# Kernel optimization log

Hardware: AMD Instinct MI355X
Metric: run time of the kernel (lower is better)

The kernel has to match this reference:

```python
import jax, jax.numpy as jnp
import numpy as np

B, S, DIM = 2, 2048, 2048
N_HEADS, N_KV_HEADS = 16, 4
HEAD_DIM = DIM // N_HEADS  # 128
N_REP = N_HEADS // N_KV_HEADS  # 4


def setup_inputs() -> dict:
    key = jax.random.key(0)
    ks = jax.random.split(key, 7)
    x = jax.random.normal(ks[0], (B, S, DIM), dtype=jnp.float32)
    cos = jax.random.uniform(ks[1], (S, HEAD_DIM // 2), dtype=jnp.float32)
    sin = jax.random.uniform(ks[2], (S, HEAD_DIM // 2), dtype=jnp.float32)
    sc = 1.0 / np.sqrt(DIM)
    wq = jax.random.normal(ks[3], (DIM, N_HEADS * HEAD_DIM), dtype=jnp.float32) * sc
    wk = jax.random.normal(ks[4], (DIM, N_KV_HEADS * HEAD_DIM), dtype=jnp.float32) * sc
    wv = jax.random.normal(ks[5], (DIM, N_KV_HEADS * HEAD_DIM), dtype=jnp.float32) * sc
    wo = jax.random.normal(ks[6], (N_HEADS * HEAD_DIM, DIM), dtype=jnp.float32) * sc
    return {"x": x, "cos": cos, "sin": sin, "wq": wq, "wk": wk, "wv": wv, "wo": wo}


def _rope(t, cos, sin):
    # t: [B, S, H, hd]; cos/sin: [S, hd/2] -> broadcast as [1, S, 1, hd/2]
    tr, ti = t[..., ::2], t[..., 1::2]
    c = cos[None, :, None, :]
    s = sin[None, :, None, :]
    out_r = tr * c - ti * s
    out_i = tr * s + ti * c
    # interleave back: stack on new last axis then flatten
    return jnp.stack([out_r, out_i], axis=-1).reshape(t.shape)


def reference(x, cos, sin, wq, wk, wv, wo):
    bsz, seqlen, _ = x.shape
    xq = (x @ wq).reshape(bsz, seqlen, N_HEADS, HEAD_DIM)
    xk = (x @ wk).reshape(bsz, seqlen, N_KV_HEADS, HEAD_DIM)
    xv = (x @ wv).reshape(bsz, seqlen, N_KV_HEADS, HEAD_DIM)
    xq = _rope(xq, cos, sin)
    xk = _rope(xk, cos, sin)
    # GQA: repeat kv heads -> [B, S, H, hd]
    xk = jnp.repeat(xk, N_REP, axis=2)
    xv = jnp.repeat(xv, N_REP, axis=2)
    scale = 1.0 / jnp.sqrt(jnp.asarray(HEAD_DIM, dtype=x.dtype))
    scores = jnp.einsum("bqhd,bkhd->bhqk", xq, xk) * scale
    causal = jnp.tril(jnp.ones((seqlen, seqlen), dtype=bool))
    scores = jnp.where(causal[None, None, :, :], scores, jnp.asarray(-jnp.inf, dtype=scores.dtype))
    attn = jax.nn.softmax(scores, axis=-1)
    out = jnp.einsum("bhqk,bkhd->bqhd", attn, xv)
    out = out.reshape(bsz, seqlen, N_HEADS * HEAD_DIM)
    return out @ wo
```

## Files before the change

### kernel.cpp

```cpp
#include <hip/hip_runtime.h>
#include <stdint.h>

#define SEQ 2048

typedef uint16_t u16;
typedef uint32_t u32;
typedef __attribute__((ext_vector_type(4))) float f32x4;
typedef __attribute__((ext_vector_type(8))) __bf16 bf16x8;
typedef __attribute__((ext_vector_type(4))) __bf16 bf16x4;

__device__ __forceinline__ u16 f2bf(float f) {
    u32 u = __float_as_uint(f);
    u += 0x7FFFu + ((u >> 16) & 1u);
    return (u16)(u >> 16);
}
__device__ __forceinline__ float bf2f(u16 h) {
    return __uint_as_float(((u32)h) << 16);
}
__device__ __forceinline__ void async16(const void* g, void* l) {
    auto gp = (__attribute__((address_space(1))) void*)const_cast<void*>(g);
    auto lp = (__attribute__((address_space(3))) void*)l;
    __builtin_amdgcn_global_load_lds(gp, lp, 16, 0, 0);
}

__global__ __launch_bounds__(256) void convert_bf16(const float* __restrict__ src,
                                                    u16* __restrict__ dst) {
    int i = blockIdx.x * 256 + threadIdx.x;
    float4 v = ((const float4*)src)[i];
    u32 lo = (u32)f2bf(v.x) | ((u32)f2bf(v.y) << 16);
    u32 hi = (u32)f2bf(v.z) | ((u32)f2bf(v.w) << 16);
    ((uint2*)dst)[i] = make_uint2(lo, hi);
}

__global__ __launch_bounds__(256) void tconv(const float* __restrict__ src,
                                             u16* __restrict__ dst, int N, int K) {
    __shared__ float tile[64][65];
    const int n0 = blockIdx.x * 64, k0 = blockIdx.y * 64;
    const int tid = threadIdx.x;
#pragma unroll
    for (int p = 0; p < 4; p++) {
        int r = p * 16 + (tid >> 4);
        int c = (tid & 15) * 4;
        float4 v = *(const float4*)&src[(size_t)(k0 + r) * N + n0 + c];
        tile[r][c] = v.x; tile[r][c+1] = v.y; tile[r][c+2] = v.z; tile[r][c+3] = v.w;
    }
    __syncthreads();
#pragma unroll
    for (int p = 0; p < 4; p++) {
        int n = p * 16 + (tid >> 4);
        int kq = (tid & 15) * 4;
        u32 lo = (u32)f2bf(tile[kq+0][n]) | ((u32)f2bf(tile[kq+1][n]) << 16);
        u32 hi = (u32)f2bf(tile[kq+2][n]) | ((u32)f2bf(tile[kq+3][n]) << 16);
        *(uint2*)&dst[(size_t)(n0 + n) * K + k0 + kq] = make_uint2(lo, hi);
    }
}

template <bool F32OUT>
__global__ __launch_bounds__(256) void gemm128(const u16* __restrict__ A,
                                               const u16* __restrict__ Bt,
                                               void* __restrict__ Cv,
                                               int M, int N, int K) {
    __shared__ u16 lA[128 * 32];
    __shared__ u16 lB[128 * 32];
    const int tid = threadIdx.x;
    const int m0 = blockIdx.y * 128, n0 = blockIdx.x * 128;
    const int lane = tid & 63;
    const int lr = lane & 15, quad = lane >> 4;
    const int w = tid >> 6;
    const int wm = (w >> 1) * 64, wn = (w & 1) * 64;

    f32x4 acc[4][4] = {};

    const int srow = tid >> 2;
    const int schunk = (tid & 3) ^ (srow & 3);
    const u16* aS0 = A  + (size_t)(m0 + srow) * K + schunk * 8;
    const u16* aS1 = aS0 + (size_t)64 * K;
    const u16* bS0 = Bt + (size_t)(n0 + srow) * K + schunk * 8;
    const u16* bS1 = bS0 + (size_t)64 * K;
    u16* lAd = lA + tid * 8;
    u16* lBd = lB + tid * 8;

    for (int k0 = 0; k0 < K; k0 += 32) {
        __syncthreads();
        async16(aS0 + k0, lAd);
        async16(aS1 + k0, lAd + 2048);
        async16(bS0 + k0, lBd);
        async16(bS1 + k0, lBd + 2048);
        __syncthreads();
        bf16x8 af[4], bfr[4];
        const int cs = (quad ^ (lr & 3)) * 8;
#pragma unroll
        for (int i = 0; i < 4; i++)
            af[i] = *(const bf16x8*)&lA[(wm + i * 16 + lr) * 32 + cs];
#pragma unroll
        for (int i = 0; i < 4; i++)
            bfr[i] = *(const bf16x8*)&lB[(wn + i * 16 + lr) * 32 + cs];
#pragma unroll
        for (int mf = 0; mf < 4; mf++)
#pragma unroll
            for (int nf = 0; nf < 4; nf++)
                acc[mf][nf] = __builtin_amdgcn_mfma_f32_16x16x32_bf16(
                    af[mf], bfr[nf], acc[mf][nf], 0, 0, 0);
    }

#pragma unroll
    for (int mf = 0; mf < 4; mf++) {
#pragma unroll
        for (int nf = 0; nf < 4; nf++) {
#pragma unroll
            for (int r = 0; r < 4; r++) {
                size_t row = (size_t)(m0 + wm + mf * 16 + quad * 4 + r);
                size_t col = (size_t)(n0 + wn + nf * 16 + lr);
                if (F32OUT)
                    ((float*)Cv)[row * (size_t)N + col] = acc[mf][nf][r];
                else
                    ((u16*)Cv)[row * (size_t)N + col] = f2bf(acc[mf][nf][r]);
            }
        }
    }
}

__global__ __launch_bounds__(256) void rope_k(u16* __restrict__ qkv,
                                              const float* __restrict__ cosp,
                                              const float* __restrict__ sinp) {
    const int t = blockIdx.x;
    const int spos = t & (SEQ - 1);
    const int tid = threadIdx.x;
    u16* row = qkv + (size_t)t * 3072;
    const int col = 2048 + 2 * tid;
    const int ci = tid & 63;
    u32 v = *(u32*)(row + col);
    float tr = bf2f((u16)(v & 0xFFFFu));
    float ti = bf2f((u16)(v >> 16));
    float cs = cosp[spos * 64 + ci];
    float sn = sinp[spos * 64 + ci];
    float orr = tr * cs - ti * sn;
    float oi  = tr * sn + ti * cs;
    *(u32*)(row + col) = (u32)f2bf(orr) | ((u32)f2bf(oi) << 16);
}

__global__ __launch_bounds__(256) void transpose_v(const u16* __restrict__ qkv,
                                                   u16* __restrict__ vt) {
    __shared__ u16 tile[64][65];
    const int bid = blockIdx.x;
    const int dt = bid & 1;
    const int st = (bid >> 1) & 31;
    const int kh = (bid >> 6) & 3;
    const int b  = bid >> 8;
    const int tid = threadIdx.x;
#pragma unroll
    for (int pp = 0; pp < 2; pp++) {
        int r  = pp * 32 + (tid >> 3);
        int c8 = (tid & 7) * 8;
        const u16* src = qkv + (size_t)(b * SEQ + st * 64 + r) * 3072 + 2560 + kh * 128 + dt * 64 + c8;
        uint4 v = *(const uint4*)src;
        tile[r][c8+0] = (u16)(v.x & 0xFFFF); tile[r][c8+1] = (u16)(v.x >> 16);
        tile[r][c8+2] = (u16)(v.y & 0xFFFF); tile[r][c8+3] = (u16)(v.y >> 16);
        tile[r][c8+4] = (u16)(v.z & 0xFFFF); tile[r][c8+5] = (u16)(v.z >> 16);
        tile[r][c8+6] = (u16)(v.w & 0xFFFF); tile[r][c8+7] = (u16)(v.w >> 16);
    }
    __syncthreads();
#pragma unroll
    for (int pp = 0; pp < 2; pp++) {
        int dr = pp * 32 + (tid >> 3);
        int s8 = (tid & 7) * 8;
        uint4 o;
        o.x = (u32)tile[s8+0][dr] | ((u32)tile[s8+1][dr] << 16);
        o.y = (u32)tile[s8+2][dr] | ((u32)tile[s8+3][dr] << 16);
        o.z = (u32)tile[s8+4][dr] | ((u32)tile[s8+5][dr] << 16);
        o.w = (u32)tile[s8+6][dr] | ((u32)tile[s8+7][dr] << 16);
        u16* dst = vt + ((size_t)((b * 4 + kh) * 128 + dt * 64 + dr)) * SEQ + st * 64 + s8;
        *(uint4*)dst = o;
    }
}

__global__ __launch_bounds__(512, 2) void flash_attn(const u16* __restrict__ qkv,
                                                     const u16* __restrict__ vt,
                                                     const float* __restrict__ cosp,
                                                     const float* __restrict__ sinp,
                                                     u16* __restrict__ ob) {
    __shared__ u16 sh[49152];
    const int bidx = blockIdx.x;
    const int a  = bidx & 7;
    const int bh = bidx >> 3;
    const int b = bh >> 4, h = bh & 15, kh = h >> 2;
    const int tid = threadIdx.x;
    const int w = tid >> 6, lane = tid & 63;
    const int grp = w >> 2, wl = w & 3;
    const int lr = lane & 15, quad = lane >> 4;
    const float qscale = 0.088388347762f * 1.4426950408889634f;

    u16* lKg = sh + grp * 16384;
    u16* lVg = lKg + 8192;
    u16* lPw = sh + 32768 + w * 2048;

    const int tidg = tid & 255;
    const int krow = tidg >> 4;
    const int kchunk = (tidg & 15) ^ krow;
    const int vrow = tidg >> 3;
    const int vchunk = (tidg & 7) ^ (vrow & 7);
    const u16* kRow = qkv + (size_t)b * SEQ * 3072 + 2048 + kh * 128
                    + (size_t)krow * 3072 + kchunk * 8;
    const u16* vRow = vt + (size_t)(b * 4 + kh) * 128 * SEQ
                    + (size_t)vrow * SEQ + vchunk * 8;
    u16* lKd = lKg + tidg * 8;
    u16* lVd = lVg + tidg * 8;

    float* mO = (float*)sh;
    float* mM = (float*)(sh + 32768);

    for (int p = 0; p < 2; p++) {
        const int qt = p ? (7 - a) : (8 + a);
        const int niters = p ? (8 - a) : (9 + a);
        const int kt0 = grp * niters;

        bf16x8 qf[2][4];
#pragma unroll
        for (int qi = 0; qi < 2; qi++) {
            const int token = qt * 128 + wl * 32 + qi * 16 + lr;
            const u16* qb = qkv + (size_t)(b * SEQ + token) * 3072 + h * 128;
#pragma unroll
            for (int kk = 0; kk < 4; kk++) {
                uint4 raw = *(const uint4*)(qb + kk * 32 + quad * 8);
                u32 rw[4] = {raw.x, raw.y, raw.z, raw.w};
                union { u16 us[8]; bf16x8 v; } fr;
#pragma unroll
                for (int pp = 0; pp < 4; pp++) {
                    int ci = kk * 16 + quad * 4 + pp;
                    float cv = cosp[token * 64 + ci];
                    float sv = sinp[token * 64 + ci];
                    float tr = bf2f((u16)(rw[pp] & 0xFFFFu));
                    float ti = bf2f((u16)(rw[pp] >> 16));
                    fr.us[2 * pp]     = f2bf((tr * cv - ti * sv) * qscale);
                    fr.us[2 * pp + 1] = f2bf((tr * sv + ti * cv) * qscale);
                }
                qf[qi][kk] = fr.v;
            }
        }

        f32x4 o[2][8] = {};
        float m_st[2] = {-1e30f, -1e30f};
        float l_st[2] = {0.f, 0.f};
        const int qg = qt * 128 + wl * 32 + lr;

        for (int t = 0; t < niters; t++) {
            const int kt = kt0 + t;
#pragma unroll
            for (int i = 0; i < 4; i++)
                async16(kRow + (size_t)(kt * 64 + i * 16) * 3072, lKd + i * 2048);
#pragma unroll
            for (int i = 0; i < 4; i++)
                async16(vRow + (size_t)(i * 32) * SEQ + kt * 64, lVd + i * 2048);
            asm volatile("s_waitcnt vmcnt(0)" ::: "memory");
            asm volatile("s_barrier" ::: "memory");

            f32x4 sc[2][4] = {};
#pragma unroll
            for (int nf = 0; nf < 4; nf++) {
#pragma unroll
                for (int kk = 0; kk < 4; kk++) {
                    bf16x8 ak = *(const bf16x8*)&lKg[(nf * 16 + lr) * 128 + (((kk * 4 + quad) ^ lr) * 8)];
                    sc[0][nf] = __builtin_amdgcn_mfma_f32_16x16x32_bf16(ak, qf[0][kk], sc[0][nf], 0, 0, 0);
                    sc[1][nf] = __builtin_amdgcn_mfma_f32_16x16x32_bf16(ak, qf[1][kk], sc[1][nf], 0, 0, 0);
                }
            }

            const int kb = kt * 64 + quad * 4;
#pragma unroll
            for (int qi = 0; qi < 2; qi++) {
                float ps[4][4];
                float mnew = m_st[qi];
                const int qrow_g = qg + qi * 16;
#pragma unroll
                for (int nf = 0; nf < 4; nf++)
#pragma unroll
                    for (int r = 0; r < 4; r++) {
                        float v = sc[qi][nf][r];
                        if ((kb + nf * 16 + r) > qrow_g) v = -1e30f;
                        ps[nf][r] = v;
                        mnew = fmaxf(mnew, v);
                    }
                mnew = fmaxf(mnew, __shfl_xor(mnew, 16));
                mnew = fmaxf(mnew, __shfl_xor(mnew, 32));
                float rsum = 0.f;
#pragma unroll
                for (int nf = 0; nf < 4; nf++)
#pragma unroll
                    for (int r = 0; r < 4; r++) {
                        float e = exp2f(ps[nf][r] - mnew);
                        ps[nf][r] = e;
                        rsum += e;
                    }
                rsum += __shfl_xor(rsum, 16);
                rsum += __shfl_xor(rsum, 32);
                float alpha = exp2f(m_st[qi] - mnew);
                l_st[qi] = l_st[qi] * alpha + rsum;
                m_st[qi] = mnew;
#pragma unroll
                for (int r = 0; r < 4; r++) {
                    float ar = __shfl(alpha, quad * 4 + r, 16);
#pragma unroll
                    for (int nd = 0; nd < 8; nd++) o[qi][nd][r] *= ar;
                }
                const int qrow = qi * 16 + lr;
#pragma unroll
                for (int nf = 0; nf < 4; nf++) {
                    u32 lo = (u32)f2bf(ps[nf][0]) | ((u32)f2bf(ps[nf][1]) << 16);
                    u32 hi = (u32)f2bf(ps[nf][2]) | ((u32)f2bf(ps[nf][3]) << 16);
                    int c = (nf * 4 + quad) ^ lr;
                    *(uint2*)&lPw[qrow * 64 + c * 4] = make_uint2(lo, hi);
                }
            }

#pragma unroll
            for (int kf = 0; kf < 2; kf++) {
                bf16x8 pa[2];
#pragma unroll
                for (int qi = 0; qi < 2; qi++) {
                    int c0 = (kf * 8 + quad * 2) ^ lr;
                    int c1 = (kf * 8 + quad * 2 + 1) ^ lr;
                    bf16x4 p0 = *(const bf16x4*)&lPw[(qi * 16 + lr) * 64 + c0 * 4];
                    bf16x4 p1 = *(const bf16x4*)&lPw[(qi * 16 + lr) * 64 + c1 * 4];
                    pa[qi] = __builtin_shufflevector(p0, p1, 0, 1, 2, 3, 4, 5, 6, 7);
                }
#pragma unroll
                for (int nd = 0; nd < 8; nd++) {
                    bf16x8 vb = *(const bf16x8*)&lVg[(nd * 16 + lr) * 64 + (((kf * 4 + quad) ^ (lr & 7)) * 8)];
                    o[0][nd] = __builtin_amdgcn_mfma_f32_16x16x32_bf16(pa[0], vb, o[0][nd], 0, 0, 0);
                    o[1][nd] = __builtin_amdgcn_mfma_f32_16x16x32_bf16(pa[1], vb, o[1][nd], 0, 0, 0);
                }
            }

            asm volatile("s_barrier" ::: "memory");
        }

        __syncthreads();
        if (grp == 1) {
#pragma unroll
            for (int qi = 0; qi < 2; qi++) {
#pragma unroll
                for (int r = 0; r < 4; r++) {
                    int row = wl * 32 + qi * 16 + quad * 4 + r;
#pragma unroll
                    for (int nd = 0; nd < 8; nd++)
                        mO[row * 128 + nd * 16 + lr] = o[qi][nd][r];
                }
                if (quad == 0) {
                    int rowl = wl * 32 + qi * 16 + lr;
                    mM[rowl * 2]     = m_st[qi];
                    mM[rowl * 2 + 1] = l_st[qi];
                }
            }
        }
        __syncthreads();
        if (grp == 0) {
#pragma unroll
            for (int qi = 0; qi < 2; qi++) {
                int rowl = wl * 32 + qi * 16 + lr;
                float m1 = mM[rowl * 2], l1 = mM[rowl * 2 + 1];
                float M  = fmaxf(m_st[qi], m1);
                float a0 = exp2f(m_st[qi] - M);
                float a1 = exp2f(m1 - M);
                float li = 1.0f / (l_st[qi] * a0 + l1 * a1);
                u16* obase = ob + (size_t)(b * SEQ + qt * 128 + wl * 32 + qi * 16) * 2048 + h * 128;
#pragma unroll
                for (int r = 0; r < 4; r++) {
                    float a0b = __shfl(a0, quad * 4 + r, 16);
                    float a1b = __shfl(a1, quad * 4 + r, 16);
                    float lib = __shfl(li, quad * 4 + r, 16);
                    int row = wl * 32 + qi * 16 + quad * 4 + r;
#pragma unroll
                    for (int nd = 0; nd < 8; nd++) {
                        float val = (o[qi][nd][r] * a0b + mO[row * 128 + nd * 16 + lr] * a1b) * lib;
                        obase[(quad * 4 + r) * 2048 + nd * 16 + lr] = f2bf(val);
                    }
                }
            }
        }
        __syncthreads();
    }
}

extern "C" void kernel_launch(void* const* d_in, const int* in_sizes, int n_in,
                              void* d_out, int out_size, void* d_ws, size_t ws_size,
                              hipStream_t stream) {
    (void)in_sizes; (void)n_in; (void)out_size; (void)ws_size;
    const float* x    = (const float*)d_in[0];
    const float* cosp = (const float*)d_in[1];
    const float* sinp = (const float*)d_in[2];
    const float* wq   = (const float*)d_in[3];
    const float* wk   = (const float*)d_in[4];
    const float* wv   = (const float*)d_in[5];
    const float* wo   = (const float*)d_in[6];
    float* out = (float*)d_out;

    char* ws = (char*)d_ws;
    u16* xb    = (u16*)(ws);
    u16* qkvb  = (u16*)(ws + (size_t)16 * 1024 * 1024);
    u16* wqkvT = (u16*)(ws + (size_t)40 * 1024 * 1024);
    u16* woT   = (u16*)(ws + (size_t)52 * 1024 * 1024);
    u16* vtb   = (u16*)(ws + (size_t)60 * 1024 * 1024);
    u16* ob    = xb;

    convert_bf16<<<8192, 256, 0, stream>>>(x, xb);
    tconv<<<dim3(32, 32), 256, 0, stream>>>(wq, wqkvT, 2048, 2048);
    tconv<<<dim3( 8, 32), 256, 0, stream>>>(wk, wqkvT + (size_t)2048 * 2048, 512, 2048);
    tconv<<<dim3( 8, 32), 256, 0, stream>>>(wv, wqkvT + (size_t)2560 * 2048, 512, 2048);
    tconv<<<dim3(32, 32), 256, 0, stream>>>(wo, woT, 2048, 2048);
    gemm128<false><<<dim3(24, 32), 256, 0, stream>>>(xb, wqkvT, (void*)qkvb, 4096, 3072, 2048);
    rope_k<<<4096, 256, 0, stream>>>(qkvb, cosp, sinp);
    transpose_v<<<512, 256, 0, stream>>>(qkvb, vtb);
    flash_attn<<<256, 512, 0, stream>>>(qkvb, vtb, cosp, sinp, ob);
    gemm128<true><<<dim3(16, 32), 256, 0, stream>>>(ob, woT, (void*)out, 4096, 2048, 2048);
}
```

Baseline: 339.5 us.

## Fuse RoPE and V-transpose into QKV GEMM epilogue, double-buffer K in attention

Merges the four weight transpose-convert launches into one kernel. The QKV GEMM epilogue now applies RoPE (with the softmax scale folded into Q) and writes V transposed through LDS, which removes the rope_k and transpose_v kernels and the per-iteration Q RoPE in attention. The flash attention kernel double-buffers K tiles with async loads and staged waitcnts, and pads the merge buffer stride. This costs more LDS, drops occupancy to one block per CU, and the epilogue now loads cos/sin per element.

```diff
diff --git a/kernel.cpp b/kernel.cpp
--- a/kernel.cpp
+++ b/kernel.cpp
@@ -22,6 +22,8 @@
     auto lp = (__attribute__((address_space(3))) void*)l;
     __builtin_amdgcn_global_load_lds(gp, lp, 16, 0, 0);
 }
+
+#define QSCALE (0.088388347762f * 1.4426950408889634f)
 
 __global__ __launch_bounds__(256) void convert_bf16(const float* __restrict__ src,
                                                     u16* __restrict__ dst) {
@@ -32,10 +34,20 @@
     ((uint2*)dst)[i] = make_uint2(lo, hi);
 }
 
-__global__ __launch_bounds__(256) void tconv(const float* __restrict__ src,
-                                             u16* __restrict__ dst, int N, int K) {
+__global__ __launch_bounds__(256) void tconv_all(const float* __restrict__ wq,
+                                                 const float* __restrict__ wk,
+                                                 const float* __restrict__ wv,
+                                                 const float* __restrict__ wo,
+                                                 u16* __restrict__ wqkvT,
+                                                 u16* __restrict__ woT) {
     __shared__ float tile[64][65];
-    const int n0 = blockIdx.x * 64, k0 = blockIdx.y * 64;
+    const int nt = blockIdx.x, kt = blockIdx.y;
+    const float* src; u16* dst; int N, nloc;
+    if (nt < 32)      { src = wq; dst = wqkvT;                        N = 2048; nloc = nt; }
+    else if (nt < 40) { src = wk; dst = wqkvT + (size_t)2048 * 2048;  N = 512;  nloc = nt - 32; }
+    else if (nt < 48) { src = wv; dst = wqkvT + (size_t)2560 * 2048;  N = 512;  nloc = nt - 40; }
+    else              { src = wo; dst = woT;                          N = 2048; nloc = nt - 48; }
+    const int n0 = nloc * 64, k0 = kt * 64;
     const int tid = threadIdx.x;
 #pragma unroll
     for (int p = 0; p < 4; p++) {
@@ -51,17 +63,21 @@
         int kq = (tid & 15) * 4;
         u32 lo = (u32)f2bf(tile[kq+0][n]) | ((u32)f2bf(tile[kq+1][n]) << 16);
         u32 hi = (u32)f2bf(tile[kq+2][n]) | ((u32)f2bf(tile[kq+3][n]) << 16);
-        *(uint2*)&dst[(size_t)(n0 + n) * K + k0 + kq] = make_uint2(lo, hi);
+        *(uint2*)&dst[(size_t)(n0 + n) * 2048 + k0 + kq] = make_uint2(lo, hi);
     }
 }
 
-template <bool F32OUT>
+template <int MODE>
 __global__ __launch_bounds__(256) void gemm128(const u16* __restrict__ A,
                                                const u16* __restrict__ Bt,
                                                void* __restrict__ Cv,
+                                               u16* __restrict__ vt,
+                                               const float* __restrict__ cosp,
+                                               const float* __restrict__ sinp,
                                                int M, int N, int K) {
-    __shared__ u16 lA[128 * 32];
-    __shared__ u16 lB[128 * 32];
+    __shared__ u16 sh[(MODE == 2) ? 16384 : 8192];
+    u16* lA = sh;
+    u16* lB = sh + 4096;
     const int tid = threadIdx.x;
     const int m0 = blockIdx.y * 128, n0 = blockIdx.x * 128;
     const int lane = tid & 63;
@@ -103,83 +119,73 @@
                     af[mf], bfr[nf], acc[mf][nf], 0, 0, 0);
     }
 
-#pragma unroll
-    for (int mf = 0; mf < 4; mf++) {
-#pragma unroll
-        for (int nf = 0; nf < 4; nf++) {
-#pragma unroll
-            for (int r = 0; r < 4; r++) {
-                size_t row = (size_t)(m0 + wm + mf * 16 + quad * 4 + r);
-                size_t col = (size_t)(n0 + wn + nf * 16 + lr);
-                if (F32OUT)
+    if (MODE == 1) {
+#pragma unroll
+        for (int mf = 0; mf < 4; mf++)
+#pragma unroll
+            for (int nf = 0; nf < 4; nf++)
+#pragma unroll
+                for (int r = 0; r < 4; r++) {
+                    size_t row = (size_t)(m0 + wm + mf * 16 + quad * 4 + r);
+                    size_t col = (size_t)(n0 + wn + nf * 16 + lr);
                     ((float*)Cv)[row * (size_t)N + col] = acc[mf][nf][r];
-                else
-                    ((u16*)Cv)[row * (size_t)N + col] = f2bf(acc[mf][nf][r]);
+                }
+    } else {
+        const int ncol0 = n0 + wn;
+        if (ncol0 < 2560) {
+            const float s2 = (ncol0 < 2048) ? QSCALE : 1.0f;
+#pragma unroll
+            for (int mf = 0; mf < 4; mf++) {
+                const int tokb = m0 + wm + mf * 16 + quad * 4;
+#pragma unroll
+                for (int nf = 0; nf < 4; nf++) {
+                    const int ci = (((ncol0 & 127) + nf * 16 + lr) >> 1);
+#pragma unroll
+                    for (int r = 0; r < 4; r++) {
+                        int tok = tokb + r;
+                        int spos = tok & (SEQ - 1);
+                        float cv = cosp[spos * 64 + ci] * s2;
+                        float sv = sinp[spos * 64 + ci] * s2;
+                        float val = acc[mf][nf][r];
+                        float par = __shfl_xor(val, 1);
+                        float outv = (lane & 1) ? fmaf(par, sv, val * cv)
+                                                : fmaf(val, cv, -par * sv);
+                        ((u16*)Cv)[(size_t)tok * 3072 + ncol0 + nf * 16 + lr] = f2bf(outv);
+                    }
+                }
+            }
+        } else {
+            __syncthreads();
+            u16* tr = sh + w * 4096;
+#pragma unroll
+            for (int mf = 0; mf < 4; mf++)
+#pragma unroll
+                for (int nf = 0; nf < 4; nf++)
+#pragma unroll
+                    for (int r = 0; r < 4; r++) {
+                        int row  = mf * 16 + quad * 4 + r;
+                        int colL = nf * 16 + lr;
+                        tr[colL * 64 + ((row + 8 * colL) & 63)] = f2bf(acc[mf][nf][r]);
+                    }
+            const int b = m0 >> 11;
+            const int s0base = (m0 & 2047) + wm;
+#pragma unroll
+            for (int i = 0; i < 8; i++) {
+                int dL = i * 8 + (lane >> 3);
+                int t0 = (lane & 7) * 8;
+                uint4 v = *(const uint4*)&tr[dL * 64 + ((t0 + 8 * dL) & 63)];
+                int dglob = (ncol0 - 2560) + dL;
+                int khh = dglob >> 7, dh = dglob & 127;
+                *(uint4*)&vt[((size_t)((b * 4 + khh) * 128 + dh)) * SEQ + s0base + t0] = v;
             }
         }
     }
 }
 
-__global__ __launch_bounds__(256) void rope_k(u16* __restrict__ qkv,
-                                              const float* __restrict__ cosp,
-                                              const float* __restrict__ sinp) {
-    const int t = blockIdx.x;
-    const int spos = t & (SEQ - 1);
-    const int tid = threadIdx.x;
-    u16* row = qkv + (size_t)t * 3072;
-    const int col = 2048 + 2 * tid;
-    const int ci = tid & 63;
-    u32 v = *(u32*)(row + col);
-    float tr = bf2f((u16)(v & 0xFFFFu));
-    float ti = bf2f((u16)(v >> 16));
-    float cs = cosp[spos * 64 + ci];
-    float sn = sinp[spos * 64 + ci];
-    float orr = tr * cs - ti * sn;
-    float oi  = tr * sn + ti * cs;
-    *(u32*)(row + col) = (u32)f2bf(orr) | ((u32)f2bf(oi) << 16);
-}
-
-__global__ __launch_bounds__(256) void transpose_v(const u16* __restrict__ qkv,
-                                                   u16* __restrict__ vt) {
-    __shared__ u16 tile[64][65];
-    const int bid = blockIdx.x;
-    const int dt = bid & 1;
-    const int st = (bid >> 1) & 31;
-    const int kh = (bid >> 6) & 3;
-    const int b  = bid >> 8;
-    const int tid = threadIdx.x;
-#pragma unroll
-    for (int pp = 0; pp < 2; pp++) {
-        int r  = pp * 32 + (tid >> 3);
-        int c8 = (tid & 7) * 8;
-        const u16* src = qkv + (size_t)(b * SEQ + st * 64 + r) * 3072 + 2560 + kh * 128 + dt * 64 + c8;
-        uint4 v = *(const uint4*)src;
-        tile[r][c8+0] = (u16)(v.x & 0xFFFF); tile[r][c8+1] = (u16)(v.x >> 16);
-        tile[r][c8+2] = (u16)(v.y & 0xFFFF); tile[r][c8+3] = (u16)(v.y >> 16);
-        tile[r][c8+4] = (u16)(v.z & 0xFFFF); tile[r][c8+5] = (u16)(v.z >> 16);
-        tile[r][c8+6] = (u16)(v.w & 0xFFFF); tile[r][c8+7] = (u16)(v.w >> 16);
-    }
-    __syncthreads();
-#pragma unroll
-    for (int pp = 0; pp < 2; pp++) {
-        int dr = pp * 32 + (tid >> 3);
-        int s8 = (tid & 7) * 8;
-        uint4 o;
-        o.x = (u32)tile[s8+0][dr] | ((u32)tile[s8+1][dr] << 16);
-        o.y = (u32)tile[s8+2][dr] | ((u32)tile[s8+3][dr] << 16);
-        o.z = (u32)tile[s8+4][dr] | ((u32)tile[s8+5][dr] << 16);
-        o.w = (u32)tile[s8+6][dr] | ((u32)tile[s8+7][dr] << 16);
-        u16* dst = vt + ((size_t)((b * 4 + kh) * 128 + dt * 64 + dr)) * SEQ + st * 64 + s8;
-        *(uint4*)dst = o;
-    }
-}
-
-__global__ __launch_bounds__(512, 2) void flash_attn(const u16* __restrict__ qkv,
+__global__ __launch_bounds__(512, 1) void flash_attn(const u16* __restrict__ qkv,
                                                      const u16* __restrict__ vt,
-                                                     const float* __restrict__ cosp,
-                                                     const float* __restrict__ sinp,
                                                      u16* __restrict__ ob) {
-    __shared__ u16 sh[49152];
+    __shared__ u16 sh[65536];
     const int bidx = blockIdx.x;
     const int a  = bidx & 7;
     const int bh = bidx >> 3;
@@ -188,11 +194,11 @@
     const int w = tid >> 6, lane = tid & 63;
     const int grp = w >> 2, wl = w & 3;
     const int lr = lane & 15, quad = lane >> 4;
-    const float qscale = 0.088388347762f * 1.4426950408889634f;
-
-    u16* lKg = sh + grp * 16384;
-    u16* lVg = lKg + 8192;
-    u16* lPw = sh + 32768 + w * 2048;
+
+    u16* kb0 = sh + grp * 24576;
+    u16* kb1 = kb0 + 8192;
+    u16* lVg = kb0 + 16384;
+    u16* lPw = sh + 49152 + w * 2048;
 
     const int tidg = tid & 255;
     const int krow = tidg >> 4;
@@ -203,11 +209,10 @@
                     + (size_t)krow * 3072 + kchunk * 8;
     const u16* vRow = vt + (size_t)(b * 4 + kh) * 128 * SEQ
                     + (size_t)vrow * SEQ + vchunk * 8;
-    u16* lKd = lKg + tidg * 8;
     u16* lVd = lVg + tidg * 8;
 
     float* mO = (float*)sh;
-    float* mM = (float*)(sh + 32768);
+    float* mM = (float*)(sh + 49152);
 
     for (int p = 0; p < 2; p++) {
         const int qt = p ? (7 - a) : (8 + a);
@@ -217,25 +222,10 @@
         bf16x8 qf[2][4];
 #pragma unroll
         for (int qi = 0; qi < 2; qi++) {
-            const int token = qt * 128 + wl * 32 + qi * 16 + lr;
-            const u16* qb = qkv + (size_t)(b * SEQ + token) * 3072 + h * 128;
-#pragma unroll
-            for (int kk = 0; kk < 4; kk++) {
-                uint4 raw = *(const uint4*)(qb + kk * 32 + quad * 8);
-                u32 rw[4] = {raw.x, raw.y, raw.z, raw.w};
-                union { u16 us[8]; bf16x8 v; } fr;
-#pragma unroll
-                for (int pp = 0; pp < 4; pp++) {
-                    int ci = kk * 16 + quad * 4 + pp;
-                    float cv = cosp[token * 64 + ci];
-                    float sv = sinp[token * 64 + ci];
-                    float tr = bf2f((u16)(rw[pp] & 0xFFFFu));
-                    float ti = bf2f((u16)(rw[pp] >> 16));
-                    fr.us[2 * pp]     = f2bf((tr * cv - ti * sv) * qscale);
-                    fr.us[2 * pp + 1] = f2bf((tr * sv + ti * cv) * qscale);
-                }
-                qf[qi][kk] = fr.v;
-            }
+            const u16* qb = qkv + (size_t)(b * SEQ + qt * 128 + wl * 32 + qi * 16 + lr) * 3072 + h * 128;
+#pragma unroll
+            for (int kk = 0; kk < 4; kk++)
+                qf[qi][kk] = *(const bf16x8*)(qb + kk * 32 + quad * 8);
         }
 
         f32x4 o[2][8] = {};
@@ -243,29 +233,43 @@
         float l_st[2] = {0.f, 0.f};
         const int qg = qt * 128 + wl * 32 + lr;
 
+        {
+            u16* d = kb0 + tidg * 8;
+#pragma unroll
+            for (int i = 0; i < 4; i++)
+                async16(kRow + (size_t)(kt0 * 64 + i * 16) * 3072, d + i * 2048);
+        }
+
         for (int t = 0; t < niters; t++) {
             const int kt = kt0 + t;
 #pragma unroll
             for (int i = 0; i < 4; i++)
-                async16(kRow + (size_t)(kt * 64 + i * 16) * 3072, lKd + i * 2048);
-#pragma unroll
-            for (int i = 0; i < 4; i++)
                 async16(vRow + (size_t)(i * 32) * SEQ + kt * 64, lVd + i * 2048);
-            asm volatile("s_waitcnt vmcnt(0)" ::: "memory");
+            if (t + 1 < niters) {
+                u16* d = ((t + 1) & 1 ? kb1 : kb0) + tidg * 8;
+#pragma unroll
+                for (int i = 0; i < 4; i++)
+                    async16(kRow + (size_t)((kt + 1) * 64 + i * 16) * 3072, d + i * 2048);
+                asm volatile("s_waitcnt vmcnt(8)" ::: "memory");
+            } else {
+                asm volatile("s_waitcnt vmcnt(4)" ::: "memory");
+            }
             asm volatile("s_barrier" ::: "memory");
 
+            const u16* lKc = (t & 1) ? kb1 : kb0;
+
             f32x4 sc[2][4] = {};
 #pragma unroll
             for (int nf = 0; nf < 4; nf++) {
 #pragma unroll
                 for (int kk = 0; kk < 4; kk++) {
-                    bf16x8 ak = *(const bf16x8*)&lKg[(nf * 16 + lr) * 128 + (((kk * 4 + quad) ^ lr) * 8)];
+                    bf16x8 ak = *(const bf16x8*)&lKc[(nf * 16 + lr) * 128 + (((kk * 4 + quad) ^ lr) * 8)];
                     sc[0][nf] = __builtin_amdgcn_mfma_f32_16x16x32_bf16(ak, qf[0][kk], sc[0][nf], 0, 0, 0);
                     sc[1][nf] = __builtin_amdgcn_mfma_f32_16x16x32_bf16(ak, qf[1][kk], sc[1][nf], 0, 0, 0);
                 }
             }
 
-            const int kb = kt * 64 + quad * 4;
+            const int kb_ = kt * 64 + quad * 4;
 #pragma unroll
             for (int qi = 0; qi < 2; qi++) {
                 float ps[4][4];
@@ -276,7 +280,7 @@
 #pragma unroll
                     for (int r = 0; r < 4; r++) {
                         float v = sc[qi][nf][r];
-                        if ((kb + nf * 16 + r) > qrow_g) v = -1e30f;
+                        if ((kb_ + nf * 16 + r) > qrow_g) v = -1e30f;
                         ps[nf][r] = v;
                         mnew = fmaxf(mnew, v);
                     }
@@ -312,6 +316,10 @@
                 }
             }
 
+            if (t + 1 < niters) asm volatile("s_waitcnt vmcnt(4)" ::: "memory");
+            else                asm volatile("s_waitcnt vmcnt(0)" ::: "memory");
+            asm volatile("s_barrier" ::: "memory");
+
 #pragma unroll
             for (int kf = 0; kf < 2; kf++) {
                 bf16x8 pa[2];
@@ -343,7 +351,7 @@
                     int row = wl * 32 + qi * 16 + quad * 4 + r;
 #pragma unroll
                     for (int nd = 0; nd < 8; nd++)
-                        mO[row * 128 + nd * 16 + lr] = o[qi][nd][r];
+                        mO[row * 132 + nd * 16 + lr] = o[qi][nd][r];
                 }
                 if (quad == 0) {
                     int rowl = wl * 32 + qi * 16 + lr;
@@ -371,7 +379,7 @@
                     int row = wl * 32 + qi * 16 + quad * 4 + r;
 #pragma unroll
                     for (int nd = 0; nd < 8; nd++) {
-                        float val = (o[qi][nd][r] * a0b + mO[row * 128 + nd * 16 + lr] * a1b) * lib;
+                        float val = (o[qi][nd][r] * a0b + mO[row * 132 + nd * 16 + lr] * a1b) * lib;
                         obase[(quad * 4 + r) * 2048 + nd * 16 + lr] = f2bf(val);
                     }
                 }
@@ -403,13 +411,10 @@
     u16* ob    = xb;
 
     convert_bf16<<<8192, 256, 0, stream>>>(x, xb);
-    tconv<<<dim3(32, 32), 256, 0, stream>>>(wq, wqkvT, 2048, 2048);
-    tconv<<<dim3( 8, 32), 256, 0, stream>>>(wk, wqkvT + (size_t)2048 * 2048, 512, 2048);
-    tconv<<<dim3( 8, 32), 256, 0, stream>>>(wv, wqkvT + (size_t)2560 * 2048, 512, 2048);
-    tconv<<<dim3(32, 32), 256, 0, stream>>>(wo, woT, 2048, 2048);
-    gemm128<false><<<dim3(24, 32), 256, 0, stream>>>(xb, wqkvT, (void*)qkvb, 4096, 3072, 2048);
-    rope_k<<<4096, 256, 0, stream>>>(qkvb, cosp, sinp);
-    transpose_v<<<512, 256, 0, stream>>>(qkvb, vtb);
-    flash_attn<<<256, 512, 0, stream>>>(qkvb, vtb, cosp, sinp, ob);
-    gemm128<true><<<dim3(16, 32), 256, 0, stream>>>(ob, woT, (void*)out, 4096, 2048, 2048);
-}
+    tconv_all<<<dim3(80, 32), 256, 0, stream>>>(wq, wk, wv, wo, wqkvT, woT);
+    gemm128<2><<<dim3(24, 32), 256, 0, stream>>>(xb, wqkvT, (void*)qkvb, vtb, cosp, sinp,
+                                                 4096, 3072, 2048);
+    flash_attn<<<256, 512, 0, stream>>>(qkvb, vtb, ob);
+    gemm128<1><<<dim3(16, 32), 256, 0, stream>>>(ob, woT, (void*)out, nullptr, nullptr, nullptr,
+                                                 4096, 2048, 2048);
+}
```

New measurement: 353.1 us. 4.0% more time.
